# Kernel tuning notes

Hardware: AMD Instinct MI355X
Metric: run time of the kernel (lower is better)

Reference implementation:

```python
import jax, jax.numpy as jnp
import numpy as np

B, LQ, LK, H = 16, 8192, 128, 128  # note LK == H is required by the final matmul
SCALE = float(np.sqrt(H))


def setup_inputs() -> dict:
    key = jax.random.key(0)
    k1, k2, k3, k4, k5, k6 = jax.random.split(key, 6)
    x1 = jax.random.normal(k1, (B, LQ, H), dtype=jnp.float32)
    x2 = jax.random.normal(k2, (B, LK, H), dtype=jnp.float32)
    x3 = jax.random.randint(k3, (B, LQ, LK), 0, 2).astype(bool)
    bound = 1.0 / np.sqrt(H)  # torch Linear default init
    wq = jax.random.uniform(k4, (H, H), minval=-bound, maxval=bound, dtype=jnp.float32)
    wk = jax.random.uniform(k5, (H, H), minval=-bound, maxval=bound, dtype=jnp.float32)
    wv = jax.random.uniform(k6, (H, H), minval=-bound, maxval=bound, dtype=jnp.float32)
    return {"x1": x1, "x2": x2, "x3": x3, "wq": wq, "wk": wk, "wv": wv}


def reference(x1, x2, x3, wq, wk, wv):
    q = x1 @ wq.T                                   # (B, Lq, H)
    k = x2 @ wk.T                                   # (B, Lk, H)
    qk = jnp.einsum('bqh,bkh->bqk', q, k) / SCALE   # (B, Lq, Lk)
    qk = jnp.where(x3, -jnp.inf, qk)                # masked_fill_ where mask is True
    attn_weight = jax.nn.softmax(qk, axis=-1)       # softmax over Lk
    v = x2 @ wv.T                                   # (B, Lk, H)
    # v @ attn_weight^T: contracts v's H axis with attn_weight's Lk axis (H == Lk)
    attn = jnp.matmul(v, jnp.swapaxes(attn_weight, -2, -1))  # (B, Lk, Lq)
    return attn
```

## Files before the change

### kernel.cpp

```cpp
#include <hip/hip_runtime.h>
#include <hip/hip_bf16.h>
#include <stdint.h>

typedef __bf16 bf16_t;
typedef __bf16 bf16x8 __attribute__((ext_vector_type(8)));
typedef float  f32x4  __attribute__((ext_vector_type(4)));
typedef float  f32x16 __attribute__((ext_vector_type(16)));
typedef unsigned int uint;
typedef uint uintx4 __attribute__((ext_vector_type(4)));

#define MFMA16(a,b,c) __builtin_amdgcn_mfma_f32_16x16x32_bf16((a),(b),(c),0,0,0)
#define MFMA32(a,b,c) __builtin_amdgcn_mfma_f32_32x32x16_bf16((a),(b),(c),0,0,0)

constexpr int NB = 16;
constexpr int LQ = 8192;
constexpr int LK = 128;
constexpr int H  = 128;

constexpr float C1 = 1.4426950408889634f / 11.313708498984761f;

constexpr size_t WS_FLAG = 0;
constexpr size_t WS_MV   = 1024;

__device__ __forceinline__ unsigned swz(unsigned row, unsigned byte) {
  return row * 256u + (byte ^ ((row & 15u) << 4));
}

__device__ __forceinline__ bf16x8 cvt_frag(const float* p) {
  f32x4 u0 = *(const f32x4*)p;
  f32x4 u1 = *(const f32x4*)(p + 4);
  bf16x8 v;
  #pragma unroll
  for (int e = 0; e < 4; ++e) { v[e] = (bf16_t)u0[e]; v[e + 4] = (bf16_t)u1[e]; }
  return v;
}

__device__ __forceinline__ f32x16 zero16() {
  f32x16 z;
  #pragma unroll
  for (int i = 0; i < 16; ++i) z[i] = 0.f;
  return z;
}

__device__ __forceinline__ uint pkbf(float a, float b) {
  uint d;
  asm("v_cvt_pk_bf16_f32 %0, %1, %2" : "=v"(d) : "v"(a), "v"(b));
  return d;
}

__global__ __launch_bounds__(512) void prep_kernel(
    const float* __restrict__ x2, const float* __restrict__ wq,
    const float* __restrict__ wk, const float* __restrict__ wv,
    const unsigned* __restrict__ x3w, uint8_t* __restrict__ ws)
{
  __shared__ uint8_t sP[131072];
  __shared__ int sF32, sBig;
  const int tid = threadIdx.x;
  const int b = blockIdx.x >> 1, which = blockIdx.x & 1;
  const int l = tid & 63, w = tid >> 6, q31 = l & 31, hi2 = l >> 5;
  uint8_t* sOut = sP + 98304;

  if (which == 0) {
    if (blockIdx.x == 0) {
      if (tid == 0) { sF32 = 0; sBig = 0; }
      __syncthreads();
      int f = 0, g = 0;
      #pragma unroll
      for (int j = 0; j < 4; ++j) {
        unsigned v = x3w[tid * 4 + j];
        if (v == 0x3f800000u) f = 1;
        else if (v > 1u) g = 1;
      }
      if (f) sF32 = 1;
      if (g) sBig = 1;
      __syncthreads();
      if (tid == 0) *(int*)(ws + WS_FLAG) = (sF32 == 0 && sBig == 1) ? 1 : 0;
    }

    {
      const int row = tid >> 2, c0 = (tid & 3) * 32;
      #pragma unroll
      for (int wh = 0; wh < 2; ++wh) {
        const float* W = wh ? wk : wq;
        uint8_t* dst = sP + wh * 32768;
        const float* s = W + row * H + c0;
        #pragma unroll
        for (int j = 0; j < 32; ++j)
          *(bf16_t*)(dst + swz(c0 + j, row * 2)) = (bf16_t)s[j];
      }
    }
    __syncthreads();

    {
      const int lo = l & 15, hi = l >> 4;
      bf16x8 a4[4];
      #pragma unroll
      for (int kk = 0; kk < 4; ++kk)
        a4[kk] = *(const bf16x8*)(sP + swz(16 * w + lo, kk * 64 + hi * 16));
      bf16_t* W2T = (bf16_t*)(sP + 65536);
      #pragma unroll
      for (int t = 0; t < 8; ++t) {
        f32x4 c = {0.f, 0.f, 0.f, 0.f};
        #pragma unroll
        for (int kk = 0; kk < 4; ++kk)
          c = MFMA16(a4[kk], *(const bf16x8*)(sP + 32768 + swz(16 * t + lo, kk * 64 + hi * 16)), c);
        #pragma unroll
        for (int r = 0; r < 4; ++r)
          W2T[(16 * w + hi * 4 + r) * H + 16 * t + lo] = (bf16_t)c[r];
      }
    }
    __syncthreads();

    if (w < 4) {
      const int wb = w;
      bf16x8 axf[8];
      const float* x2r = x2 + ((size_t)b * LK + 32 * wb + q31) * H;
      #pragma unroll
      for (int kt = 0; kt < 8; ++kt)
        axf[kt] = cvt_frag(x2r + kt * 16 + 8 * hi2);
      const bf16_t* W2Tl = (const bf16_t*)(sP + 65536);
      #pragma unroll
      for (int nt = 0; nt < 4; ++nt) {
        f32x16 c = zero16();
        #pragma unroll
        for (int kt = 0; kt < 8; ++kt)
          c = MFMA32(axf[kt],
                     *(const bf16x8*)(W2Tl + (size_t)(nt * 32 + q31) * H + kt * 16 + 8 * hi2), c);
        #pragma unroll
        for (int r = 0; r < 16; ++r)
          *(bf16_t*)(sOut + swz(32 * wb + (r & 3) + 8 * (r >> 2) + 4 * hi2,
                                (nt * 32 + q31) * 2)) = (bf16_t)c[r];
      }
    }
  } else {
    if (w < 4) {
      const int wb = w;
      bf16x8 axf[8];
      const float* x2r = x2 + ((size_t)b * LK + 32 * wb + q31) * H;
      #pragma unroll
      for (int kt = 0; kt < 8; ++kt)
        axf[kt] = cvt_frag(x2r + kt * 16 + 8 * hi2);
      #pragma unroll
      for (int nt = 0; nt < 4; ++nt) {
        f32x16 c = zero16();
        #pragma unroll
        for (int kt = 0; kt < 8; ++kt)
          c = MFMA32(axf[kt],
                     cvt_frag(wv + (size_t)(nt * 32 + q31) * H + kt * 16 + 8 * hi2), c);
        #pragma unroll
        for (int r = 0; r < 16; ++r)
          *(bf16_t*)(sOut + swz(32 * wb + (r & 3) + 8 * (r >> 2) + 4 * hi2,
                                (nt * 32 + q31) * 2)) = (bf16_t)c[r];
      }
    }
  }
  __syncthreads();

  {
    uint8_t* dst = ws + WS_MV + (size_t)b * 65536 + (size_t)which * 32768;
    #pragma unroll
    for (int pass = 0; pass < 4; ++pass) {
      const int idx = tid + pass * 512;
      const int chunk = idx >> 6, le = idx & 63;
      const int t4 = chunk >> 3, kt = chunk & 7;
      bf16x8 v = *(const bf16x8*)(sOut + swz(t4 * 32 + (le & 31),
                                             kt * 32 + (le >> 5) * 16));
      *(bf16x8*)(dst + (size_t)idx * 16) = v;
    }
  }
}

__global__ __launch_bounds__(256, 4) void attn_kernel(
    const float* __restrict__ x1, const void* __restrict__ x3,
    const uint8_t* __restrict__ ws, float* __restrict__ out)
{
  const int tid = threadIdx.x, blk = blockIdx.x;
  const int b = blk >> 6, qc = (blk & 63) * 128;
  const int l = tid & 63, w4 = tid >> 6;
  const int q31 = l & 31, hi2 = l >> 5;
  const int byteMode = *(const int*)(ws + WS_FLAG);

  const int q0w = qc + w4 * 32;
  const size_t qrow = (size_t)b * LQ + q0w + q31;

  const uint8_t* Mf = ws + WS_MV + (size_t)b * 65536;
  const uint8_t* Vf = Mf + 32768;

  f32x4 xr[16];
  {
    const float* xp = x1 + qrow * H;
    #pragma unroll
    for (int kt = 0; kt < 8; ++kt) {
      xr[2 * kt]     = *(const f32x4*)(xp + kt * 16 + 8 * hi2);
      xr[2 * kt + 1] = *(const f32x4*)(xp + kt * 16 + 8 * hi2 + 4);
    }
  }

  uint mu[16];
  if (byteMode) {
    const uint8_t* mp = (const uint8_t*)x3 + qrow * LK;
    #pragma unroll
    for (int jt = 0; jt < 4; ++jt)
      #pragma unroll
      for (int rg = 0; rg < 4; ++rg)
        mu[jt * 4 + rg] = *(const uint*)(mp + jt * 32 + 8 * rg + 4 * hi2);
  }

  bf16x8 xbf[8];
  #pragma unroll
  for (int kt = 0; kt < 8; ++kt)
    #pragma unroll
    for (int e = 0; e < 4; ++e) {
      xbf[kt][e]     = (bf16_t)xr[2 * kt][e];
      xbf[kt][e + 4] = (bf16_t)xr[2 * kt + 1][e];
    }

  const uint* mrowW = (const uint*)x3 + qrow * LK;
  bf16x8 pb[8];

  #pragma unroll
  for (int half = 0; half < 2; ++half) {
    const int jt0 = half * 2, jt1 = half * 2 + 1;
    f32x16 s0 = zero16(), s1 = zero16();
    __builtin_amdgcn_s_setprio(1);
    #pragma unroll
    for (int kt = 0; kt < 8; ++kt) {
      s0 = MFMA32(*(const bf16x8*)(Mf + (((jt0 * 8 + kt) << 10) | (l << 4))),
                  xbf[kt], s0);
      s1 = MFMA32(*(const bf16x8*)(Mf + (((jt1 * 8 + kt) << 10) | (l << 4))),
                  xbf[kt], s1);
    }
    __builtin_amdgcn_s_setprio(0);

    #pragma unroll
    for (int jj = 0; jj < 2; ++jj) {
      f32x16& sj = jj ? s1 : s0;
      const int jt = half * 2 + jj;
      #pragma unroll
      for (int rg = 0; rg < 4; ++rg) {
        uint m0, m1, m2, m3;
        if (byteMode) {
          uint u = mu[jt * 4 + rg];
          m0 = u & 0xffu; m1 = (u >> 8) & 0xffu; m2 = (u >> 16) & 0xffu; m3 = u >> 24;
        } else {
          uint4 mw = *(const uint4*)(mrowW + jt * 32 + 8 * rg + 4 * hi2);
          m0 = mw.x; m1 = mw.y; m2 = mw.z; m3 = mw.w;
        }
        float p0 = __builtin_amdgcn_exp2f(sj[rg * 4 + 0] * C1);
        float p1 = __builtin_amdgcn_exp2f(sj[rg * 4 + 1] * C1);
        float p2 = __builtin_amdgcn_exp2f(sj[rg * 4 + 2] * C1);
        float p3 = __builtin_amdgcn_exp2f(sj[rg * 4 + 3] * C1);
        sj[rg * 4 + 0] = m0 ? 0.f : p0;
        sj[rg * 4 + 1] = m1 ? 0.f : p1;
        sj[rg * 4 + 2] = m2 ? 0.f : p2;
        sj[rg * 4 + 3] = m3 ? 0.f : p3;
      }

      #pragma unroll
      for (int h = 0; h < 2; ++h) {
        uint A = pkbf(sj[h * 8 + 0], sj[h * 8 + 1]);
        uint C = pkbf(sj[h * 8 + 2], sj[h * 8 + 3]);
        uint B = pkbf(sj[h * 8 + 4], sj[h * 8 + 5]);
        uint D = pkbf(sj[h * 8 + 6], sj[h * 8 + 7]);
        asm("v_permlane32_swap_b32 %0, %1" : "+v"(A), "+v"(B));
        asm("v_permlane32_swap_b32 %0, %1" : "+v"(C), "+v"(D));
        uintx4 t; t.x = A; t.y = C; t.z = B; t.w = D;
        pb[jt * 2 + h] = __builtin_bit_cast(bf16x8, t);
      }
    }
  }

  bf16x8 ones1;
  #pragma unroll
  for (int e = 0; e < 8; ++e) ones1[e] = (bf16_t)1.f;

  f32x16 dacc = zero16();
  {
    f32x16 o0 = zero16(), o1 = zero16();
    __builtin_amdgcn_s_setprio(1);
    #pragma unroll
    for (int kt = 0; kt < 8; ++kt) {
      dacc = MFMA32(ones1, pb[kt], dacc);
      o0 = MFMA32(*(const bf16x8*)(Vf + (((0 * 8 + kt) << 10) | (l << 4))), pb[kt], o0);
      o1 = MFMA32(*(const bf16x8*)(Vf + (((1 * 8 + kt) << 10) | (l << 4))), pb[kt], o1);
    }
    __builtin_amdgcn_s_setprio(0);
    const float inv = 1.0f / dacc[0];
    #pragma unroll
    for (int r = 0; r < 16; ++r) {
      const int ibase = (r & 3) + 8 * (r >> 2) + 4 * hi2;
      out[((size_t)b * LK + ibase) * LQ + q0w + q31] = o0[r] * inv;
      out[((size_t)b * LK + 32 + ibase) * LQ + q0w + q31] = o1[r] * inv;
    }
  }

  {
    f32x16 o2 = zero16(), o3 = zero16();
    __builtin_amdgcn_s_setprio(1);
    #pragma unroll
    for (int kt = 0; kt < 8; ++kt) {
      o2 = MFMA32(*(const bf16x8*)(Vf + (((2 * 8 + kt) << 10) | (l << 4))), pb[kt], o2);
      o3 = MFMA32(*(const bf16x8*)(Vf + (((3 * 8 + kt) << 10) | (l << 4))), pb[kt], o3);
    }
    __builtin_amdgcn_s_setprio(0);
    const float inv = 1.0f / dacc[0];
    #pragma unroll
    for (int r = 0; r < 16; ++r) {
      const int ibase = (r & 3) + 8 * (r >> 2) + 4 * hi2;
      out[((size_t)b * LK + 64 + ibase) * LQ + q0w + q31] = o2[r] * inv;
      out[((size_t)b * LK + 96 + ibase) * LQ + q0w + q31] = o3[r] * inv;
    }
  }
}

extern "C" void kernel_launch(void* const* d_in, const int* in_sizes, int n_in,
                              void* d_out, int out_size, void* d_ws, size_t ws_size,
                              hipStream_t stream) {
  const float* x1 = (const float*)d_in[0];
  const float* x2 = (const float*)d_in[1];
  const void*  x3 = d_in[2];
  const float* wq = (const float*)d_in[3];
  const float* wk = (const float*)d_in[4];
  const float* wv = (const float*)d_in[5];
  uint8_t* ws = (uint8_t*)d_ws;
  float* out = (float*)d_out;

  prep_kernel<<<2 * NB, 512, 0, stream>>>(x2, wq, wk, wv, (const unsigned*)x3, ws);
  attn_kernel<<<NB * (LQ / 128), 256, 0, stream>>>(x1, x3, ws, out);
}
```

Baseline: 51.15 us.

## Stage x1 and mask tiles into LDS via global_load_lds with XOR swizzle

Replaces the per-lane strided global loads of x1 rows and mask bytes with coalesced 16-byte global_load_lds transfers into swizzled shared memory. Lanes then read their MFMA operand slices and mask words back from LDS. The fp32-to-bf16 conversion now uses packed cvt instructions. This should improve global access coalescing and cut register pressure. In exchange it uses 80KB of LDS per block and lowers the occupancy hint from 4 to 2 blocks per CU.

```diff
diff --git a/kernel.cpp b/kernel.cpp
--- a/kernel.cpp
+++ b/kernel.cpp
@@ -46,6 +46,12 @@
   uint d;
   asm("v_cvt_pk_bf16_f32 %0, %1, %2" : "=v"(d) : "v"(a), "v"(b));
   return d;
+}
+
+__device__ __forceinline__ void gl16(const void* g, void* l) {
+  __builtin_amdgcn_global_load_lds(
+      (const __attribute__((address_space(1))) uint32_t*)g,
+      (__attribute__((address_space(3))) uint32_t*)l, 16, 0, 0);
 }
 
 __global__ __launch_bounds__(512) void prep_kernel(
@@ -170,10 +176,13 @@
   }
 }
 
-__global__ __launch_bounds__(256, 4) void attn_kernel(
+__global__ __launch_bounds__(256, 2) void attn_kernel(
     const float* __restrict__ x1, const void* __restrict__ x3,
     const uint8_t* __restrict__ ws, float* __restrict__ out)
 {
+  __shared__ uint8_t sX[65536];
+  __shared__ uint8_t sMk[16384];
+
   const int tid = threadIdx.x, blk = blockIdx.x;
   const int b = blk >> 6, qc = (blk & 63) * 128;
   const int l = tid & 63, w4 = tid >> 6;
@@ -186,34 +195,45 @@
   const uint8_t* Mf = ws + WS_MV + (size_t)b * 65536;
   const uint8_t* Vf = Mf + 32768;
 
-  f32x4 xr[16];
   {
-    const float* xp = x1 + qrow * H;
-    #pragma unroll
-    for (int kt = 0; kt < 8; ++kt) {
-      xr[2 * kt]     = *(const f32x4*)(xp + kt * 16 + 8 * hi2);
-      xr[2 * kt + 1] = *(const f32x4*)(xp + kt * 16 + 8 * hi2 + 4);
-    }
-  }
-
-  uint mu[16];
-  if (byteMode) {
-    const uint8_t* mp = (const uint8_t*)x3 + qrow * LK;
-    #pragma unroll
-    for (int jt = 0; jt < 4; ++jt)
-      #pragma unroll
-      for (int rg = 0; rg < 4; ++rg)
-        mu[jt * 4 + rg] = *(const uint*)(mp + jt * 32 + 8 * rg + 4 * hi2);
-  }
-
+    const uint8_t* xgb = (const uint8_t*)(x1 + ((size_t)b * LQ + qc) * H);
+    #pragma unroll
+    for (int j = 0; j < 16; ++j) {
+      const int off = w4 * 16384 + j * 1024 + l * 16;
+      const int row = off >> 9;
+      const int wb  = off & 511;
+      gl16(xgb + row * 512 + (wb ^ ((row & 31) << 4)), sX + off);
+    }
+    if (byteMode) {
+      const uint8_t* mgb = (const uint8_t*)x3 + ((size_t)b * LQ + qc) * LK;
+      #pragma unroll
+      for (int j = 0; j < 4; ++j) {
+        const int off = w4 * 4096 + j * 1024 + l * 16;
+        const int row = off >> 7;
+        const int wb  = off & 127;
+        gl16(mgb + row * 128 + (wb ^ ((row & 7) << 4)), sMk + off);
+      }
+    }
+  }
+  asm volatile("s_waitcnt vmcnt(0)" ::: "memory");
+
+  const int xrow = w4 * 32 + q31;
+  const uint8_t* xls = sX + xrow * 512;
+  const uint xxor = (uint)(xrow & 31) << 4;
   bf16x8 xbf[8];
   #pragma unroll
-  for (int kt = 0; kt < 8; ++kt)
-    #pragma unroll
-    for (int e = 0; e < 4; ++e) {
-      xbf[kt][e]     = (bf16_t)xr[2 * kt][e];
-      xbf[kt][e + 4] = (bf16_t)xr[2 * kt + 1][e];
-    }
+  for (int kt = 0; kt < 8; ++kt) {
+    const uint colb = kt * 64 + hi2 * 32;
+    f32x4 a0 = *(const f32x4*)(xls + (colb ^ xxor));
+    f32x4 a1 = *(const f32x4*)(xls + ((colb + 16) ^ xxor));
+    uintx4 t;
+    t.x = pkbf(a0[0], a0[1]); t.y = pkbf(a0[2], a0[3]);
+    t.z = pkbf(a1[0], a1[1]); t.w = pkbf(a1[2], a1[3]);
+    xbf[kt] = __builtin_bit_cast(bf16x8, t);
+  }
+
+  const uint8_t* mls = sMk + xrow * 128;
+  const uint mxor = (uint)(xrow & 7) << 4;
 
   const uint* mrowW = (const uint*)x3 + qrow * LK;
   bf16x8 pb[8];
@@ -240,7 +260,8 @@
       for (int rg = 0; rg < 4; ++rg) {
         uint m0, m1, m2, m3;
         if (byteMode) {
-          uint u = mu[jt * 4 + rg];
+          const uint colm = (uint)(jt * 32 + 8 * rg + 4 * hi2);
+          uint u = *(const uint*)(mls + (colm ^ mxor));
           m0 = u & 0xffu; m1 = (u >> 8) & 0xffu; m2 = (u >> 16) & 0xffu; m3 = u >> 24;
         } else {
           uint4 mw = *(const uint4*)(mrowW + jt * 32 + 8 * rg + 4 * hi2);
```

Result: slower. 57.27 us (+12.0%).
